# Kernel optimization log

Hardware: AMD Instinct MI355X
Metric: run time of the kernel (lower is better)

## Reference

```python
import jax, jax.numpy as jnp
import numpy as np

MAX_DISTANCE = 10
N_OUT = 8


def setup_inputs() -> dict:
    key = jax.random.key(0)
    k1, k2 = jax.random.split(key)
    B, N = 32, 512
    adjacency = jax.random.uniform(k1, (B, N, N), dtype=jnp.float32)
    node_mask = jnp.ones((B, N), dtype=bool)
    emb = jax.random.normal(k2, (MAX_DISTANCE + 2, N_OUT), dtype=jnp.float32)
    return {"adjacency": adjacency, "node_mask": node_mask, "emb": emb}


def _shortest_path_indices(adjacency, node_mask):
    """All-pairs BFS distances up to MAX_DISTANCE via frontier matmuls.

    Returns int32 (B, N, N): d in [0, MAX_DISTANCE] if reachable within
    MAX_DISTANCE hops, else MAX_DISTANCE + 1 (also for invalid node pairs).
    """
    B, N, _ = adjacency.shape
    adj = adjacency > 0.5
    adj = adj | jnp.swapaxes(adj, -1, -2)  # symmetrize
    valid_pair = node_mask[:, :, None] & node_mask[:, None, :]
    adj = (adj & valid_pair).astype(jnp.float32)  # (B, N, N)

    eye = jnp.eye(N, dtype=bool)[None]
    reach0 = eye & valid_pair  # dist 0 only on valid diagonal
    dist0 = jnp.where(reach0, 0, MAX_DISTANCE + 1).astype(jnp.int32)

    def step(carry, t):
        reach, dist = carry
        expanded = jnp.matmul(reach.astype(jnp.float32), adj) > 0  # one BFS hop
        newly = expanded & ~reach
        dist = jnp.where(newly, t.astype(jnp.int32), dist)
        return (reach | newly, dist), None

    (_, dist), _ = jax.lax.scan(step, (reach0, dist0), jnp.arange(1, MAX_DISTANCE + 1))
    return dist


def reference(adjacency, node_mask, emb):
    dist = _shortest_path_indices(adjacency, node_mask)  # (B, N, N)
    return emb[dist]  # (B, N, N, n_out)
```

## Files before the change

### kernel.cpp

```cpp
#include <hip/hip_runtime.h>

#define NODES 512
#define WORDS 16
#define NBATCH 32
#define SENTINEL 11
#define NEMB 12
#define NOUT 8
#define G 4

__global__ void __launch_bounds__(256)
pack_bits(const float* __restrict__ A, const int* __restrict__ mask,
          unsigned int* __restrict__ bitA) {
    const int tid = blockIdx.x * 256 + threadIdx.x;
    const int t = threadIdx.x;
    const int w = tid & 15;
    const int i = (tid >> 4) & 511;
    const int b = tid >> 13;

    __shared__ unsigned int s_mw[WORDS];
    {
        bool m0 = mask[b * NODES + t] != 0;
        bool m1 = mask[b * NODES + 256 + t] != 0;
        unsigned long long b0 = __ballot(m0);
        unsigned long long b1 = __ballot(m1);
        if ((t & 63) == 0) {
            int wv = t >> 6;
            s_mw[2 * wv]         = (unsigned int)b0;
            s_mw[2 * wv + 1]     = (unsigned int)(b0 >> 32);
            s_mw[8 + 2 * wv]     = (unsigned int)b1;
            s_mw[8 + 2 * wv + 1] = (unsigned int)(b1 >> 32);
        }
    }

    const float4* p = (const float4*)(A + (size_t)tid * 32);
    unsigned int bits = 0;
#pragma unroll
    for (int q = 0; q < 8; ++q) {
        float4 v = p[q];
        bits |= (v.x > 0.5f ? 1u : 0u) << (4 * q);
        bits |= (v.y > 0.5f ? 1u : 0u) << (4 * q + 1);
        bits |= (v.z > 0.5f ? 1u : 0u) << (4 * q + 2);
        bits |= (v.w > 0.5f ? 1u : 0u) << (4 * q + 3);
    }
    __syncthreads();
    bool rv = (s_mw[i >> 5] >> (i & 31)) & 1u;
    bitA[tid] = rv ? (bits & s_mw[w]) : 0u;
}

__global__ void __launch_bounds__(256)
symmetrize(const unsigned int* __restrict__ bitA, unsigned int* __restrict__ adjb) {
    int tid = blockIdx.x * 256 + threadIdx.x;
    int w = tid & 15;
    int i = (tid >> 4) & 511;
    int b = tid >> 13;
    const unsigned int* base = bitA + (size_t)b * NODES * WORDS;
    unsigned int word = base[i * WORDS + w];
    unsigned int t = 0;
    int iw = i >> 5, ib = i & 31;
#pragma unroll
    for (int k = 0; k < 32; ++k) {
        t |= ((base[(32 * w + k) * WORDS + iw] >> ib) & 1u) << k;
    }
    adjb[tid] = word | t;
}

__global__ void __launch_bounds__(512, 8)
bfs_store(const unsigned int* __restrict__ adjb, const int* __restrict__ mask,
          const float* __restrict__ emb, float4* __restrict__ out4) {
    const int i0 = blockIdx.x * G;
    const int b = blockIdx.y;
    const int j = threadIdx.x;

    __shared__ unsigned int s_adj[NODES][WORDS];
    __shared__ unsigned int s_f[2][G][WORDS];
    __shared__ unsigned int s_state[2][8];
    __shared__ unsigned int s_dist[NODES];
    __shared__ __align__(16) float s_emb[NEMB * NOUT];

    if (j < NEMB * NOUT) s_emb[j] = emb[j];

    {
        const uint4* rowp = (const uint4*)(adjb + ((size_t)b * NODES + j) * WORDS);
        uint4* dst = (uint4*)&s_adj[j][0];
        dst[0] = rowp[0]; dst[1] = rowp[1]; dst[2] = rowp[2]; dst[3] = rowp[3];
    }

    const bool valid_j = (mask[b * NODES + j] != 0);

    if (j < G * WORDS) {
        int s = j >> 4, w = j & 15;
        int i = i0 + s;
        bool v = (mask[b * NODES + i] != 0);
        s_f[0][s][w] = (v && (i >> 5) == w) ? (1u << (i & 31)) : 0u;
    }

    unsigned int dists = 0x0B0B0B0Bu;
    unsigned int reachm = 0;
#pragma unroll
    for (int s = 0; s < G; ++s) {
        if ((j == i0 + s) && valid_j) {
            dists &= ~(0xffu << (8 * s));
            reachm |= 1u << s;
        }
    }
    __syncthreads();

    int p = 0;
    for (int t = 1; t <= 10; ++t) {
        const uint4* a4 = (const uint4*)&s_adj[j][0];
        uint4 a0 = a4[0], a1 = a4[1], a2 = a4[2], a3 = a4[3];
        unsigned int newm = 0;
#pragma unroll
        for (int s = 0; s < G; ++s) {
            const uint4* f4 = (const uint4*)s_f[p][s];
            uint4 f0 = f4[0], f1 = f4[1], f2 = f4[2], f3 = f4[3];
            unsigned int hit =
                (a0.x & f0.x) | (a0.y & f0.y) | (a0.z & f0.z) | (a0.w & f0.w) |
                (a1.x & f1.x) | (a1.y & f1.y) | (a1.z & f1.z) | (a1.w & f1.w) |
                (a2.x & f2.x) | (a2.y & f2.y) | (a2.z & f2.z) | (a2.w & f2.w) |
                (a3.x & f3.x) | (a3.y & f3.y) | (a3.z & f3.z) | (a3.w & f3.w);
            if (hit && !((reachm >> s) & 1u)) newm |= 1u << s;
        }
        unsigned long long anyb = 0;
        unsigned long long doneb = ~0ull;
#pragma unroll
        for (int s = 0; s < G; ++s) {
            unsigned long long bal = __ballot((newm >> s) & 1u);
            anyb |= bal;
            doneb &= __ballot((((reachm | newm) >> s) & 1u) || !valid_j);
            if ((j & 63) == 0) {
                int wv = j >> 6;
                s_f[p ^ 1][s][2 * wv]     = (unsigned int)bal;
                s_f[p ^ 1][s][2 * wv + 1] = (unsigned int)(bal >> 32);
            }
        }
#pragma unroll
        for (int s = 0; s < G; ++s) {
            if ((newm >> s) & 1u)
                dists = (dists & ~(0xffu << (8 * s))) | ((unsigned int)t << (8 * s));
        }
        reachm |= newm;
        if ((j & 63) == 0) {
            s_state[p ^ 1][j >> 6] =
                ((anyb != 0ull) ? 1u : 0u) | ((doneb == ~0ull) ? 2u : 0u);
        }
        __syncthreads();
        p ^= 1;
        unsigned int anyw = 0, donew = 2;
#pragma unroll
        for (int wv = 0; wv < 8; ++wv) {
            unsigned int st = s_state[p][wv];
            anyw |= st;
            donew &= st;
        }
        if (!(anyw & 1u) || (donew & 2u)) break;
    }

    s_dist[j] = dists;
    __syncthreads();

    const float4* e4 = (const float4*)s_emb;
    unsigned int dw0 = s_dist[j >> 1];
    unsigned int dw1 = s_dist[256 + (j >> 1)];
    const int half = j & 1;
    size_t base0 = ((size_t)b * NODES + i0) * (NODES * NOUT / 4);
#pragma unroll
    for (int s = 0; s < G; ++s) {
        int d0 = (dw0 >> (8 * s)) & 0xff;
        int d1 = (dw1 >> (8 * s)) & 0xff;
        out4[base0 + (size_t)s * 1024 + j]       = e4[2 * d0 + half];
        out4[base0 + (size_t)s * 1024 + 512 + j] = e4[2 * d1 + half];
    }
}

extern "C" void kernel_launch(void* const* d_in, const int* in_sizes, int n_in,
                              void* d_out, int out_size, void* d_ws, size_t ws_size,
                              hipStream_t stream) {
    const float* adjacency = (const float*)d_in[0];
    const int* node_mask = (const int*)d_in[1];
    const float* emb = (const float*)d_in[2];
    float4* out4 = (float4*)d_out;

    unsigned int* bitA = (unsigned int*)d_ws;
    unsigned int* adjb = bitA + (size_t)NBATCH * NODES * WORDS;

    pack_bits<<<1024, 256, 0, stream>>>(adjacency, node_mask, bitA);
    symmetrize<<<1024, 256, 0, stream>>>(bitA, adjb);
    bfs_store<<<dim3(NODES / G, NBATCH), 512, 0, stream>>>(adjb, node_mask, emb, out4);
}
```

Baseline: 83.51 us.

## Halve source rows per block and keep adjacency row in registers

Each block now handles two source nodes instead of four, which doubles the grid. Each thread keeps its packed adjacency row in registers for all BFS steps instead of staging it in 32 KB of shared memory. The per-step ballots for the frontier and the termination state are merged into one warp-leader write. Less shared memory per block should allow more blocks per CU and more parallelism for the store-heavy epilogue. In exchange, every block re-reads the full 32 KB adjacency of its batch, doubling global/L2 read traffic.

```diff
diff --git a/kernel.cpp b/kernel.cpp
--- a/kernel.cpp
+++ b/kernel.cpp
@@ -6,7 +6,7 @@
 #define SENTINEL 11
 #define NEMB 12
 #define NOUT 8
-#define G 4
+#define G 2
 
 __global__ void __launch_bounds__(256)
 pack_bits(const float* __restrict__ A, const int* __restrict__ mask,
@@ -71,7 +71,6 @@
     const int b = blockIdx.y;
     const int j = threadIdx.x;
 
-    __shared__ unsigned int s_adj[NODES][WORDS];
     __shared__ unsigned int s_f[2][G][WORDS];
     __shared__ unsigned int s_state[2][8];
     __shared__ unsigned int s_dist[NODES];
@@ -79,11 +78,8 @@
 
     if (j < NEMB * NOUT) s_emb[j] = emb[j];
 
-    {
-        const uint4* rowp = (const uint4*)(adjb + ((size_t)b * NODES + j) * WORDS);
-        uint4* dst = (uint4*)&s_adj[j][0];
-        dst[0] = rowp[0]; dst[1] = rowp[1]; dst[2] = rowp[2]; dst[3] = rowp[3];
-    }
+    const uint4* rowp = (const uint4*)(adjb + ((size_t)b * NODES + j) * WORDS);
+    uint4 ar0 = rowp[0], ar1 = rowp[1], ar2 = rowp[2], ar3 = rowp[3];
 
     const bool valid_j = (mask[b * NODES + j] != 0);
 
@@ -94,7 +90,7 @@
         s_f[0][s][w] = (v && (i >> 5) == w) ? (1u << (i & 31)) : 0u;
     }
 
-    unsigned int dists = 0x0B0B0B0Bu;
+    unsigned int dists = 0x0B0Bu;
     unsigned int reachm = 0;
 #pragma unroll
     for (int s = 0; s < G; ++s) {
@@ -107,32 +103,30 @@
 
     int p = 0;
     for (int t = 1; t <= 10; ++t) {
-        const uint4* a4 = (const uint4*)&s_adj[j][0];
-        uint4 a0 = a4[0], a1 = a4[1], a2 = a4[2], a3 = a4[3];
         unsigned int newm = 0;
 #pragma unroll
         for (int s = 0; s < G; ++s) {
             const uint4* f4 = (const uint4*)s_f[p][s];
             uint4 f0 = f4[0], f1 = f4[1], f2 = f4[2], f3 = f4[3];
             unsigned int hit =
-                (a0.x & f0.x) | (a0.y & f0.y) | (a0.z & f0.z) | (a0.w & f0.w) |
-                (a1.x & f1.x) | (a1.y & f1.y) | (a1.z & f1.z) | (a1.w & f1.w) |
-                (a2.x & f2.x) | (a2.y & f2.y) | (a2.z & f2.z) | (a2.w & f2.w) |
-                (a3.x & f3.x) | (a3.y & f3.y) | (a3.z & f3.z) | (a3.w & f3.w);
+                (ar0.x & f0.x) | (ar0.y & f0.y) | (ar0.z & f0.z) | (ar0.w & f0.w) |
+                (ar1.x & f1.x) | (ar1.y & f1.y) | (ar1.z & f1.z) | (ar1.w & f1.w) |
+                (ar2.x & f2.x) | (ar2.y & f2.y) | (ar2.z & f2.z) | (ar2.w & f2.w) |
+                (ar3.x & f3.x) | (ar3.y & f3.y) | (ar3.z & f3.z) | (ar3.w & f3.w);
             if (hit && !((reachm >> s) & 1u)) newm |= 1u << s;
         }
-        unsigned long long anyb = 0;
-        unsigned long long doneb = ~0ull;
-#pragma unroll
-        for (int s = 0; s < G; ++s) {
-            unsigned long long bal = __ballot((newm >> s) & 1u);
-            anyb |= bal;
-            doneb &= __ballot((((reachm | newm) >> s) & 1u) || !valid_j);
-            if ((j & 63) == 0) {
-                int wv = j >> 6;
-                s_f[p ^ 1][s][2 * wv]     = (unsigned int)bal;
-                s_f[p ^ 1][s][2 * wv + 1] = (unsigned int)(bal >> 32);
-            }
+        unsigned long long bal0 = __ballot(newm & 1u);
+        unsigned long long bal1 = __ballot((newm >> 1) & 1u);
+        bool alldone = (((reachm | newm) == 3u) || !valid_j);
+        unsigned long long balD = __ballot(alldone);
+        if ((j & 63) == 0) {
+            int wv = j >> 6;
+            s_f[p ^ 1][0][2 * wv]     = (unsigned int)bal0;
+            s_f[p ^ 1][0][2 * wv + 1] = (unsigned int)(bal0 >> 32);
+            s_f[p ^ 1][1][2 * wv]     = (unsigned int)bal1;
+            s_f[p ^ 1][1][2 * wv + 1] = (unsigned int)(bal1 >> 32);
+            s_state[p ^ 1][wv] = (((bal0 | bal1) != 0ull) ? 1u : 0u) |
+                                 ((balD == ~0ull) ? 2u : 0u);
         }
 #pragma unroll
         for (int s = 0; s < G; ++s) {
@@ -140,10 +134,6 @@
                 dists = (dists & ~(0xffu << (8 * s))) | ((unsigned int)t << (8 * s));
         }
         reachm |= newm;
-        if ((j & 63) == 0) {
-            s_state[p ^ 1][j >> 6] =
-                ((anyb != 0ull) ? 1u : 0u) | ((doneb == ~0ull) ? 2u : 0u);
-        }
         __syncthreads();
         p ^= 1;
         unsigned int anyw = 0, donew = 2;
```

New measurement: 79.14 us (median of 2 runs). 1.06x faster.

## Compute BFS distances 1 and 2 directly from adjacency rows, doubling sources per block

Applied to the files above, without the earlier changes.

The BFS kernel now handles 8 source nodes per block with 256 threads, each owning two target columns. It no longer stages the full adjacency matrix in shared memory. Distances 0, 1 and 2 come straight from the source rows: a direct bit test gives distance 1, and an AND of source and target rows gives distance 2. The frontier loop runs from hop 3 only when needed. For dense graphs this skips the shared-memory adjacency load and most BFS iterations, at the cost of more registers, adjacency rows read from global memory, and fewer blocks.

```diff
diff --git a/kernel.cpp b/kernel.cpp
--- a/kernel.cpp
+++ b/kernel.cpp
@@ -6,7 +6,7 @@
 #define SENTINEL 11
 #define NEMB 12
 #define NOUT 8
-#define G 4
+#define G 8
 
 __global__ void __launch_bounds__(256)
 pack_bits(const float* __restrict__ A, const int* __restrict__ mask,
@@ -64,112 +64,204 @@
     adjb[tid] = word | t;
 }
 
-__global__ void __launch_bounds__(512, 8)
+__global__ void __launch_bounds__(256, 8)
 bfs_store(const unsigned int* __restrict__ adjb, const int* __restrict__ mask,
           const float* __restrict__ emb, float4* __restrict__ out4) {
     const int i0 = blockIdx.x * G;
     const int b = blockIdx.y;
-    const int j = threadIdx.x;
-
-    __shared__ unsigned int s_adj[NODES][WORDS];
+    const int t = threadIdx.x;
+    const int cA = t, cB = t + 256;
+
+    __shared__ unsigned int s_rowi[G][WORDS];
+    __shared__ unsigned int s_dw0[NODES];
+    __shared__ unsigned int s_dw1[NODES];
     __shared__ unsigned int s_f[2][G][WORDS];
-    __shared__ unsigned int s_state[2][8];
-    __shared__ unsigned int s_dist[NODES];
+    __shared__ unsigned int s_state[2][4];
     __shared__ __align__(16) float s_emb[NEMB * NOUT];
 
-    if (j < NEMB * NOUT) s_emb[j] = emb[j];
-
-    {
-        const uint4* rowp = (const uint4*)(adjb + ((size_t)b * NODES + j) * WORDS);
-        uint4* dst = (uint4*)&s_adj[j][0];
-        dst[0] = rowp[0]; dst[1] = rowp[1]; dst[2] = rowp[2]; dst[3] = rowp[3];
-    }
-
-    const bool valid_j = (mask[b * NODES + j] != 0);
-
-    if (j < G * WORDS) {
-        int s = j >> 4, w = j & 15;
-        int i = i0 + s;
-        bool v = (mask[b * NODES + i] != 0);
-        s_f[0][s][w] = (v && (i >> 5) == w) ? (1u << (i & 31)) : 0u;
-    }
-
-    unsigned int dists = 0x0B0B0B0Bu;
-    unsigned int reachm = 0;
-#pragma unroll
-    for (int s = 0; s < G; ++s) {
-        if ((j == i0 + s) && valid_j) {
-            dists &= ~(0xffu << (8 * s));
-            reachm |= 1u << s;
-        }
-    }
-    __syncthreads();
-
-    int p = 0;
-    for (int t = 1; t <= 10; ++t) {
-        const uint4* a4 = (const uint4*)&s_adj[j][0];
-        uint4 a0 = a4[0], a1 = a4[1], a2 = a4[2], a3 = a4[3];
-        unsigned int newm = 0;
-#pragma unroll
-        for (int s = 0; s < G; ++s) {
-            const uint4* f4 = (const uint4*)s_f[p][s];
-            uint4 f0 = f4[0], f1 = f4[1], f2 = f4[2], f3 = f4[3];
+    if (t < NEMB * NOUT) s_emb[t] = emb[t];
+
+    const unsigned int* Ab = adjb + (size_t)b * NODES * WORDS;
+    if (t < G * 4) {
+        int s = t >> 2, q = t & 3;
+        ((uint4*)s_rowi[s])[q] = ((const uint4*)(Ab + (size_t)(i0 + s) * WORDS))[q];
+    }
+
+    bool vs[G];
+#pragma unroll
+    for (int s = 0; s < G; ++s) vs[s] = (mask[b * NODES + i0 + s] != 0);
+    const bool validA = (mask[b * NODES + cA] != 0);
+    const bool validB = (mask[b * NODES + cB] != 0);
+
+    const uint4* rA = (const uint4*)(Ab + (size_t)cA * WORDS);
+    const uint4* rB = (const uint4*)(Ab + (size_t)cB * WORDS);
+
+    __syncthreads();
+
+    unsigned int dwA0 = 0, dwA1 = 0, dwB0 = 0, dwB1 = 0;
+    {
+        uint4 r0 = rA[0], r1 = rA[1], r2 = rA[2], r3 = rA[3];
+#pragma unroll
+        for (int s = 0; s < G; ++s) {
+            const uint4* R = (const uint4*)s_rowi[s];
+            uint4 R0 = R[0], R1 = R[1], R2 = R[2], R3 = R[3];
             unsigned int hit =
-                (a0.x & f0.x) | (a0.y & f0.y) | (a0.z & f0.z) | (a0.w & f0.w) |
-                (a1.x & f1.x) | (a1.y & f1.y) | (a1.z & f1.z) | (a1.w & f1.w) |
-                (a2.x & f2.x) | (a2.y & f2.y) | (a2.z & f2.z) | (a2.w & f2.w) |
-                (a3.x & f3.x) | (a3.y & f3.y) | (a3.z & f3.z) | (a3.w & f3.w);
-            if (hit && !((reachm >> s) & 1u)) newm |= 1u << s;
-        }
-        unsigned long long anyb = 0;
-        unsigned long long doneb = ~0ull;
-#pragma unroll
-        for (int s = 0; s < G; ++s) {
-            unsigned long long bal = __ballot((newm >> s) & 1u);
-            anyb |= bal;
-            doneb &= __ballot((((reachm | newm) >> s) & 1u) || !valid_j);
-            if ((j & 63) == 0) {
-                int wv = j >> 6;
-                s_f[p ^ 1][s][2 * wv]     = (unsigned int)bal;
-                s_f[p ^ 1][s][2 * wv + 1] = (unsigned int)(bal >> 32);
-            }
-        }
-#pragma unroll
-        for (int s = 0; s < G; ++s) {
-            if ((newm >> s) & 1u)
-                dists = (dists & ~(0xffu << (8 * s))) | ((unsigned int)t << (8 * s));
-        }
-        reachm |= newm;
-        if ((j & 63) == 0) {
-            s_state[p ^ 1][j >> 6] =
-                ((anyb != 0ull) ? 1u : 0u) | ((doneb == ~0ull) ? 2u : 0u);
-        }
-        __syncthreads();
-        p ^= 1;
-        unsigned int anyw = 0, donew = 2;
-#pragma unroll
-        for (int wv = 0; wv < 8; ++wv) {
-            unsigned int st = s_state[p][wv];
-            anyw |= st;
-            donew &= st;
-        }
-        if (!(anyw & 1u) || (donew & 2u)) break;
-    }
-
-    s_dist[j] = dists;
+                (r0.x & R0.x) | (r0.y & R0.y) | (r0.z & R0.z) | (r0.w & R0.w) |
+                (r1.x & R1.x) | (r1.y & R1.y) | (r1.z & R1.z) | (r1.w & R1.w) |
+                (r2.x & R2.x) | (r2.y & R2.y) | (r2.z & R2.z) | (r2.w & R2.w) |
+                (r3.x & R3.x) | (r3.y & R3.y) | (r3.z & R3.z) | (r3.w & R3.w);
+            unsigned int bit1 = (s_rowi[s][cA >> 5] >> (cA & 31)) & 1u;
+            unsigned int d = (cA == i0 + s && vs[s]) ? 0u
+                             : (bit1 ? 1u : (hit ? 2u : (unsigned)SENTINEL));
+            if (s < 4) dwA0 |= d << (8 * s); else dwA1 |= d << (8 * (s - 4));
+        }
+        s_dw0[cA] = dwA0; s_dw1[cA] = dwA1;
+    }
+    {
+        uint4 r0 = rB[0], r1 = rB[1], r2 = rB[2], r3 = rB[3];
+#pragma unroll
+        for (int s = 0; s < G; ++s) {
+            const uint4* R = (const uint4*)s_rowi[s];
+            uint4 R0 = R[0], R1 = R[1], R2 = R[2], R3 = R[3];
+            unsigned int hit =
+                (r0.x & R0.x) | (r0.y & R0.y) | (r0.z & R0.z) | (r0.w & R0.w) |
+                (r1.x & R1.x) | (r1.y & R1.y) | (r1.z & R1.z) | (r1.w & R1.w) |
+                (r2.x & R2.x) | (r2.y & R2.y) | (r2.z & R2.z) | (r2.w & R2.w) |
+                (r3.x & R3.x) | (r3.y & R3.y) | (r3.z & R3.z) | (r3.w & R3.w);
+            unsigned int bit1 = (s_rowi[s][cB >> 5] >> (cB & 31)) & 1u;
+            unsigned int d = (cB == i0 + s && vs[s]) ? 0u
+                             : (bit1 ? 1u : (hit ? 2u : (unsigned)SENTINEL));
+            if (s < 4) dwB0 |= d << (8 * s); else dwB1 |= d << (8 * (s - 4));
+        }
+        s_dw0[cB] = dwB0; s_dw1[cB] = dwB1;
+    }
+
+    {
+        bool thr_done =
+            (!validA || (((dwA0 | (dwA0 >> 16)) & 0x0808u) == 0 &&
+                         ((dwA1 | (dwA1 >> 16)) & 0x0808u) == 0)) &&
+            (!validB || (((dwB0 | (dwB0 >> 16)) & 0x0808u) == 0 &&
+                         ((dwB1 | (dwB1 >> 16)) & 0x0808u) == 0));
+        unsigned long long balD = __ballot(thr_done);
+        unsigned long long anyAcc = 0;
+#pragma unroll
+        for (int s = 0; s < G; ++s) {
+            unsigned int dA = ((s < 4 ? dwA0 >> (8 * s) : dwA1 >> (8 * (s - 4))) & 0xffu);
+            unsigned int dB = ((s < 4 ? dwB0 >> (8 * s) : dwB1 >> (8 * (s - 4))) & 0xffu);
+            unsigned long long fA = __ballot(dA == 2u);
+            unsigned long long fB = __ballot(dB == 2u);
+            anyAcc |= fA | fB;
+            if ((t & 63) == 0) {
+                int wv = t >> 6;
+                s_f[0][s][2 * wv]         = (unsigned int)fA;
+                s_f[0][s][2 * wv + 1]     = (unsigned int)(fA >> 32);
+                s_f[0][s][8 + 2 * wv]     = (unsigned int)fB;
+                s_f[0][s][8 + 2 * wv + 1] = (unsigned int)(fB >> 32);
+            }
+        }
+        if ((t & 63) == 0)
+            s_state[0][t >> 6] = ((anyAcc != 0ull) ? 1u : 0u) |
+                                 ((balD == ~0ull) ? 2u : 0u);
+    }
+    __syncthreads();
+    unsigned int anyw = 0, donew = 2;
+#pragma unroll
+    for (int wv = 0; wv < 4; ++wv) {
+        unsigned int st = s_state[0][wv];
+        anyw |= st; donew &= st;
+    }
+
+    if ((anyw & 1u) && !(donew & 2u)) {
+        unsigned int reachA = 0, reachB = 0;
+#pragma unroll
+        for (int s = 0; s < G; ++s) {
+            unsigned int dA = ((s < 4 ? dwA0 >> (8 * s) : dwA1 >> (8 * (s - 4))) & 0xffu);
+            unsigned int dB = ((s < 4 ? dwB0 >> (8 * s) : dwB1 >> (8 * (s - 4))) & 0xffu);
+            if (dA != (unsigned)SENTINEL) reachA |= 1u << s;
+            if (dB != (unsigned)SENTINEL) reachB |= 1u << s;
+        }
+        int p = 0;
+        for (int tt = 3; tt <= 10; ++tt) {
+            uint4 a0 = rA[0], a1 = rA[1], a2 = rA[2], a3 = rA[3];
+            uint4 b0 = rB[0], b1 = rB[1], b2 = rB[2], b3 = rB[3];
+            unsigned int newA = 0, newB = 0;
+#pragma unroll
+            for (int s = 0; s < G; ++s) {
+                const uint4* F = (const uint4*)s_f[p][s];
+                uint4 f0 = F[0], f1 = F[1], f2 = F[2], f3 = F[3];
+                unsigned int hA =
+                    (a0.x & f0.x) | (a0.y & f0.y) | (a0.z & f0.z) | (a0.w & f0.w) |
+                    (a1.x & f1.x) | (a1.y & f1.y) | (a1.z & f1.z) | (a1.w & f1.w) |
+                    (a2.x & f2.x) | (a2.y & f2.y) | (a2.z & f2.z) | (a2.w & f2.w) |
+                    (a3.x & f3.x) | (a3.y & f3.y) | (a3.z & f3.z) | (a3.w & f3.w);
+                unsigned int hB =
+                    (b0.x & f0.x) | (b0.y & f0.y) | (b0.z & f0.z) | (b0.w & f0.w) |
+                    (b1.x & f1.x) | (b1.y & f1.y) | (b1.z & f1.z) | (b1.w & f1.w) |
+                    (b2.x & f2.x) | (b2.y & f2.y) | (b2.z & f2.z) | (b2.w & f2.w) |
+                    (b3.x & f3.x) | (b3.y & f3.y) | (b3.z & f3.z) | (b3.w & f3.w);
+                if (hA && !((reachA >> s) & 1u)) newA |= 1u << s;
+                if (hB && !((reachB >> s) & 1u)) newB |= 1u << s;
+            }
+            unsigned long long anyAcc = 0;
+#pragma unroll
+            for (int s = 0; s < G; ++s) {
+                unsigned long long nA = __ballot((newA >> s) & 1u);
+                unsigned long long nB = __ballot((newB >> s) & 1u);
+                anyAcc |= nA | nB;
+                if ((t & 63) == 0) {
+                    int wv = t >> 6;
+                    s_f[p ^ 1][s][2 * wv]         = (unsigned int)nA;
+                    s_f[p ^ 1][s][2 * wv + 1]     = (unsigned int)(nA >> 32);
+                    s_f[p ^ 1][s][8 + 2 * wv]     = (unsigned int)nB;
+                    s_f[p ^ 1][s][8 + 2 * wv + 1] = (unsigned int)(nB >> 32);
+                }
+            }
+            bool dn = (!validA || ((reachA | newA) == 0xffu)) &&
+                      (!validB || ((reachB | newB) == 0xffu));
+            unsigned long long bD = __ballot(dn);
+            if ((t & 63) == 0)
+                s_state[p ^ 1][t >> 6] = ((anyAcc != 0ull) ? 1u : 0u) |
+                                         ((bD == ~0ull) ? 2u : 0u);
+#pragma unroll
+            for (int s = 0; s < G; ++s) {
+                if ((newA >> s) & 1u) {
+                    if (s < 4) dwA0 = (dwA0 & ~(0xffu << (8 * s))) | ((unsigned)tt << (8 * s));
+                    else       dwA1 = (dwA1 & ~(0xffu << (8 * (s - 4)))) | ((unsigned)tt << (8 * (s - 4)));
+                }
+                if ((newB >> s) & 1u) {
+                    if (s < 4) dwB0 = (dwB0 & ~(0xffu << (8 * s))) | ((unsigned)tt << (8 * s));
+                    else       dwB1 = (dwB1 & ~(0xffu << (8 * (s - 4)))) | ((unsigned)tt << (8 * (s - 4)));
+                }
+            }
+            reachA |= newA; reachB |= newB;
+            __syncthreads();
+            p ^= 1;
+            unsigned int aw = 0, dw = 2;
+#pragma unroll
+            for (int wv = 0; wv < 4; ++wv) {
+                unsigned int st = s_state[p][wv];
+                aw |= st; dw &= st;
+            }
+            if (!(aw & 1u) || (dw & 2u)) break;
+        }
+        s_dw0[cA] = dwA0; s_dw1[cA] = dwA1;
+        s_dw0[cB] = dwB0; s_dw1[cB] = dwB1;
+    }
     __syncthreads();
 
     const float4* e4 = (const float4*)s_emb;
-    unsigned int dw0 = s_dist[j >> 1];
-    unsigned int dw1 = s_dist[256 + (j >> 1)];
-    const int half = j & 1;
     size_t base0 = ((size_t)b * NODES + i0) * (NODES * NOUT / 4);
 #pragma unroll
-    for (int s = 0; s < G; ++s) {
-        int d0 = (dw0 >> (8 * s)) & 0xff;
-        int d1 = (dw1 >> (8 * s)) & 0xff;
-        out4[base0 + (size_t)s * 1024 + j]       = e4[2 * d0 + half];
-        out4[base0 + (size_t)s * 1024 + 512 + j] = e4[2 * d1 + half];
+    for (int q = 0; q < 4; ++q) {
+        int k = t + 256 * q;
+        int half = k & 1;
+        unsigned int w0 = s_dw0[k >> 1];
+        unsigned int w1 = s_dw1[k >> 1];
+#pragma unroll
+        for (int s = 0; s < G; ++s) {
+            int d = (int)((s < 4 ? w0 >> (8 * s) : w1 >> (8 * (s - 4))) & 0xffu);
+            out4[base0 + (size_t)s * 1024 + k] = e4[2 * d + half];
+        }
     }
 }
 
@@ -186,5 +278,5 @@
 
     pack_bits<<<1024, 256, 0, stream>>>(adjacency, node_mask, bitA);
     symmetrize<<<1024, 256, 0, stream>>>(bitA, adjb);
-    bfs_store<<<dim3(NODES / G, NBATCH), 512, 0, stream>>>(adjb, node_mask, emb, out4);
-}
+    bfs_store<<<dim3(NODES / G, NBATCH), 256, 0, stream>>>(adjb, node_mask, emb, out4);
+}
```

Result: slower. 148.3 us (+77.6%).
